# Performance work log

Measured on AMD Instinct MI355X. Metric: run time of the kernel, lower is better.

## Reference

```python
import jax, jax.numpy as jnp
import numpy as np

B, N, E, F, H, OUT = 128, 2048, 16384, 32, 64, 16


def setup_inputs() -> dict:
    key = jax.random.key(0)
    ks = jax.random.split(key, 8)
    node_features = jax.random.normal(ks[0], (B, N, F), jnp.float32)
    edge_index = jax.random.randint(ks[1], (B, 2, E), 0, N)
    n_nodes = jax.random.randint(ks[2], (B,), N // 2, N + 1)
    # prefix node mask (required for the original's index-consistency)
    node_mask = jnp.arange(N)[None, :] < n_nodes[:, None]
    glorot = lambda k, sh, fan: jax.random.normal(k, sh, jnp.float32) / np.sqrt(fan)
    return dict(
        node_features=node_features, edge_index=edge_index, node_mask=node_mask,
        W1=glorot(ks[3], (F, H), F), b1=jnp.zeros((H,), jnp.float32),
        W2=glorot(ks[4], (H, H), H), b2=jnp.zeros((H,), jnp.float32),
        aW1=glorot(ks[5], (H, H), H), ab1=jnp.zeros((H,), jnp.float32),
        aW2=glorot(ks[6], (H, OUT), H), ab2=jnp.zeros((OUT,), jnp.float32),
    )


def reference(node_features, edge_index, node_mask, W1, b1, W2, b2, aW1, ab1, aW2, ab2):
    x = node_features
    src, dst = edge_index[:, 0], edge_index[:, 1]          # [B,E] source->target
    n = node_mask.sum(-1)                                   # [B] valid nodes per graph
    max_idx = n - 1
    emask = (src <= max_idx[:, None]) & (dst <= max_idx[:, None])
    w = emask.astype(x.dtype)                               # [B,E] edge weights

    # flatten batch into one big segment space [B*N]
    offs = (jnp.arange(B, dtype=src.dtype) * N)[:, None]
    src_f = (src + offs).reshape(-1)
    dst_f = (dst + offs).reshape(-1)
    w_f = w.reshape(-1)

    # GCN normalization with self-loops (PyG GCNConv default)
    deg = jax.ops.segment_sum(w_f, dst_f, num_segments=B * N).reshape(B, N)
    deg = deg + node_mask.astype(x.dtype)                   # self-loop weight 1 on valid nodes
    dis = jnp.where(deg > 0, jax.lax.rsqrt(deg), 0.0)       # deg^{-1/2}, [B,N]
    dis_f = dis.reshape(-1)
    norm = dis_f[src_f] * dis_f[dst_f] * w_f                # [B*E]
    nmask_f = node_mask.reshape(-1).astype(x.dtype)[:, None]
    nmask = node_mask.astype(x.dtype)[..., None]

    def gcn_relu(h, W, bias):
        hW = (h @ W).reshape(B * N, -1)                     # transform first (PyG order)
        msgs = hW[src_f] * norm[:, None]                    # [B*E, H]
        agg = jax.ops.segment_sum(msgs, dst_f, num_segments=B * N)
        agg = agg + hW * ((dis * dis).reshape(-1)[:, None] * nmask_f)  # self-loop term
        out = (agg.reshape(B, N, -1) + bias) * nmask
        return jax.nn.relu(out)

    h1 = gcn_relu(x * nmask, W1, b1)
    h2 = gcn_relu(h1, W2, b2)

    # mean pool over valid nodes (zeros if empty graph)
    pooled = h2.sum(1) / jnp.maximum(n, 1)[:, None].astype(x.dtype)
    hidden = jax.nn.relu(pooled @ aW1 + ab1)
    logits = hidden @ aW2 + ab2                             # [B, OUT]
    return logits
```

## Files before the change

### kernel.cpp

```cpp
#include <hip/hip_runtime.h>
#include <hip/hip_bf16.h>

#define B 128
#define N 2048
#define E 16384
#define F 32
#define H 64
#define OUTD 16
#define CAP 16
#define NP1 (N + 1)

typedef __attribute__((ext_vector_type(8))) short bf16x8;
typedef __attribute__((ext_vector_type(4))) float f32x4;

__device__ __forceinline__ float b2f(unsigned short u) {
    return __uint_as_float(((unsigned int)u) << 16);
}
__device__ __forceinline__ unsigned short f2b(float f) {
    unsigned int x = __float_as_uint(f);
    unsigned int r = (x + 0x7FFFu + ((x >> 16) & 1u)) >> 16;
    return (unsigned short)r;
}
__device__ __forceinline__ unsigned int pack2(float a, float b) {
    return (unsigned int)f2b(a) | ((unsigned int)f2b(b) << 16);
}

__device__ __forceinline__ void unpack8(float (&a)[8], uint4 u) {
    a[0] += __uint_as_float(u.x << 16);
    a[1] += __uint_as_float(u.x & 0xffff0000u);
    a[2] += __uint_as_float(u.y << 16);
    a[3] += __uint_as_float(u.y & 0xffff0000u);
    a[4] += __uint_as_float(u.z << 16);
    a[5] += __uint_as_float(u.z & 0xffff0000u);
    a[6] += __uint_as_float(u.w << 16);
    a[7] += __uint_as_float(u.w & 0xffff0000u);
}

struct PrepArgs {
    const void* src[9];
    void* dst[9];
};

__global__ __launch_bounds__(1024) void k_build(
    const void* __restrict__ x, const int* __restrict__ eidx,
    const void* __restrict__ mask, PrepArgs pa, int* __restrict__ flags,
    int* __restrict__ n_arr, float* __restrict__ dis,
    unsigned char* __restrict__ degc, unsigned short* __restrict__ ssrc,
    int2* __restrict__ ovf, int* __restrict__ ovf_cnt,
    float* __restrict__ pooled, unsigned int* __restrict__ y_u,
    unsigned int* __restrict__ z_u) {
    __shared__ int s_cnt[N];
    __shared__ float s_fred[16];
    __shared__ int s_w[16];
    __shared__ int s_n, s_ovf, s_xbf, s_pf;
    const int b = blockIdx.x;
    const int t = threadIdx.x;
    const int bN = b * N;
    {
        const unsigned short* p = (const unsigned short*)x;
        float s = fminf(fabsf(b2f(p[t])), 1e6f);
        for (int o = 32; o > 0; o >>= 1) s += __shfl_down(s, o);
        if ((t & 63) == 0) s_fred[t >> 6] = s;
        __syncthreads();
        if (t == 0) {
            float a = 0.f;
            for (int i = 0; i < 16; i++) a += s_fred[i];
            int f = (a < 100.0f * 1024.0f) ? 1 : 0;
            s_xbf = f;
            if (b == 0) flags[0] = f;
        }
    }
    const unsigned char* mb = (const unsigned char*)mask;
    int mode;
    if (mb[0] == 0x80 && mb[1] == 0x3F) mode = 2;
    else if (mb[0] != 0 && mb[1] != 0) mode = 0;
    else if (mb[0] != 0) mode = (mb[4] != 0) ? 1 : 4;
    else mode = 3;
    int cnt = 0;
    if (mode == 0) {
        const unsigned char* r = mb + (size_t)b * N;
        for (int i = t; i < N; i += 1024) cnt += (r[i] != 0);
    } else if (mode == 1 || mode == 3) {
        const unsigned int* r = (const unsigned int*)mask + (size_t)b * N;
        for (int i = t; i < N; i += 1024) cnt += (r[i] != 0);
    } else if (mode == 2) {
        const unsigned short* r = (const unsigned short*)mask + (size_t)b * N;
        for (int i = t; i < N; i += 1024) cnt += (r[i] != 0);
    } else {
        const unsigned long long* r = (const unsigned long long*)mask + (size_t)b * N;
        for (int i = t; i < N; i += 1024) cnt += (r[i] != 0ULL);
    }
    for (int o = 32; o > 0; o >>= 1) cnt += __shfl_down(cnt, o);
    if ((t & 63) == 0) s_w[t >> 6] = cnt;
    for (int i = t; i < N; i += 1024) s_cnt[i] = 0;
    {
        const int4 iv = make_int4(0x08000800, 0x08000800, 0x08000800, 0x08000800);
        int4* sp4 = (int4*)(ssrc + (size_t)bN * CAP);
        for (int i = t; i < N * CAP / 8; i += 1024) sp4[i] = iv;
    }
    if (t < 16) y_u[((size_t)b * NP1 + N) * (F / 2) + t] = 0u;
    if (t >= 32 && t < 64) z_u[((size_t)b * NP1 + N) * (H / 2) + (t - 32)] = 0u;
    if (t == 0) s_ovf = 0;
    __syncthreads();
    if (t == 0) {
        int a = 0;
        for (int i = 0; i < 16; i++) a += s_w[i];
        s_n = a > N ? N : a;
    }
    __syncthreads();
    const int n = s_n;
    const int4* es4 = (const int4*)(eidx + (size_t)b * 2 * E);
    const int4* ed4 = es4 + E / 4;
    for (int i = t; i < E / 4; i += 1024) {
        int4 s4 = es4[i], d4 = ed4[i];
#define FILL1(SS, DD)                                                          \
        if ((unsigned)(SS) < (unsigned)n && (unsigned)(DD) < (unsigned)n) {    \
            int pos = atomicAdd(&s_cnt[DD], 1);                                \
            if (pos < CAP)                                                     \
                ssrc[((size_t)(bN + (DD))) * CAP + pos] = (unsigned short)(SS);\
            else {                                                             \
                int oi = atomicAdd(&s_ovf, 1);                                 \
                if (oi < E) ovf[(size_t)b * E + oi] = make_int2((DD), (SS));   \
            }                                                                  \
        }
        FILL1(s4.x, d4.x) FILL1(s4.y, d4.y) FILL1(s4.z, d4.z) FILL1(s4.w, d4.w)
#undef FILL1
    }
    __syncthreads();
    for (int v = t; v < N; v += 1024) {
        int c = s_cnt[v];
        dis[bN + v] = (v < n) ? rsqrtf((float)(c + 1)) : 0.0f;
        degc[bN + v] = (unsigned char)(c < CAP ? c : CAP);
    }
    if (t < H) pooled[b * H + t] = 0.0f;
    if (t == 0) { n_arr[b] = n; ovf_cnt[b] = s_ovf; }
    if (s_xbf) {
        const uint4* xp = (const uint4*)((const unsigned short*)x + (size_t)bN * F);
        for (int i = t; i < N * 4; i += 1024) {
            const int v = i >> 2;
            const int c = s_cnt[v];
            const float dv = (v < n) ? rsqrtf((float)(c + 1)) : 0.0f;
            uint4 u = xp[i];
            uint4 o;
            o.x = pack2(b2f((unsigned short)u.x) * dv, b2f((unsigned short)(u.x >> 16)) * dv);
            o.y = pack2(b2f((unsigned short)u.y) * dv, b2f((unsigned short)(u.y >> 16)) * dv);
            o.z = pack2(b2f((unsigned short)u.z) * dv, b2f((unsigned short)(u.z >> 16)) * dv);
            o.w = pack2(b2f((unsigned short)u.w) * dv, b2f((unsigned short)(u.w >> 16)) * dv);
            *(uint4*)(y_u + ((size_t)b * NP1 + v) * (F / 2) + (i & 3) * 4) = o;
        }
    } else {
        const float4* xp = (const float4*)((const float*)x + (size_t)bN * F);
        for (int i = t; i < N * 4; i += 1024) {
            const int v = i >> 2;
            const int c = s_cnt[v];
            const float dv = (v < n) ? rsqrtf((float)(c + 1)) : 0.0f;
            float4 v1 = xp[i * 2], v2 = xp[i * 2 + 1];
            uint4 o;
            o.x = pack2(v1.x * dv, v1.y * dv);
            o.y = pack2(v1.z * dv, v1.w * dv);
            o.z = pack2(v2.x * dv, v2.y * dv);
            o.w = pack2(v2.z * dv, v2.w * dv);
            *(uint4*)(y_u + ((size_t)b * NP1 + v) * (F / 2) + (i & 3) * 4) = o;
        }
    }
    if (b >= 1 && b <= 8) {
        int sz;
        switch (b) {
            case 1: sz = F * H; break;
            case 2: sz = H; break;
            case 3: sz = H * H; break;
            case 4: sz = H; break;
            case 5: sz = H * H; break;
            case 6: sz = H; break;
            case 7: sz = H * OUTD; break;
            default: sz = OUTD; break;
        }
        const int K = sz < 1024 ? sz : 1024;
        const unsigned short* p = (const unsigned short*)pa.src[b];
        float s = (t < K) ? fminf(fabsf(b2f(p[t])), 1e6f) : 0.f;
        for (int o = 32; o > 0; o >>= 1) s += __shfl_down(s, o);
        __syncthreads();
        if ((t & 63) == 0) s_fred[t >> 6] = s;
        __syncthreads();
        if (t == 0) {
            float a = 0.f;
            for (int i = 0; i < 16; i++) a += s_fred[i];
            s_pf = (a < 100.0f * (float)K) ? 1 : 0;
        }
        __syncthreads();
        const int fl = s_pf;
        auto rd = [&](int i) -> float {
            return fl ? b2f(((const unsigned short*)pa.src[b])[i])
                      : ((const float*)pa.src[b])[i];
        };
        if (b == 1) {
            unsigned short* dst = (unsigned short*)pa.dst[b];
            for (int i = t; i < F * H; i += 1024) {
                int k = i >> 6, n2 = i & 63;
                dst[n2 * 40 + k] = f2b(rd(i));
            }
        } else if (b == 3) {
            unsigned short* dst = (unsigned short*)pa.dst[b];
            for (int i = t; i < H * H; i += 1024) {
                int k = i >> 6, n2 = i & 63;
                dst[n2 * 72 + k] = f2b(rd(i));
            }
        } else {
            float* dst = (float*)pa.dst[b];
            for (int i = t; i < sz; i += 1024) dst[i] = rd(i);
        }
    }
}

__global__ __launch_bounds__(256) void k_agg_gemm1(
    const unsigned int* __restrict__ y_u, const float* __restrict__ dis,
    const unsigned char* __restrict__ degc, const unsigned short* __restrict__ ssrc,
    const int2* __restrict__ ovf, const int* __restrict__ ovf_cnt,
    const unsigned short* __restrict__ w1t, const float* __restrict__ b1f,
    unsigned short* __restrict__ zs) {
    __shared__ unsigned short s_e[64 * CAP];
    __shared__ unsigned char s_dg[64];
    __shared__ float s_dv[64];
    __shared__ float s_b1[64];
    __shared__ __align__(16) unsigned short s_w1t[64 * 40];
    __shared__ __align__(16) unsigned short s_a1[64 * 40];
    const int bid = blockIdx.x;
    const int b = (bid & 7) + ((bid >> 8) << 3);
    const int v0 = ((bid >> 3) & 31) * 64;
    const int t = threadIdx.x;
    const int bN = b * N;
    if (t < 128) ((int4*)s_e)[t] = ((const int4*)(ssrc + (size_t)(bN + v0) * CAP))[t];
    if (t >= 128 && t < 144)
        ((unsigned int*)s_dg)[t - 128] = ((const unsigned int*)(degc + bN + v0))[t - 128];
    if (t >= 192) s_dv[t - 192] = dis[bN + v0 + (t - 192)];
    if (t >= 144 && t < 208) s_b1[t - 144] = b1f[t - 144];
    for (int i = t; i < 320; i += 256) ((int4*)s_w1t)[i] = ((const int4*)w1t)[i];
    __syncthreads();
    const int lane = t & 63;
    const int w = t >> 6;
    const int oc = ovf_cnt[b];
    const unsigned int* yb = y_u + (size_t)b * NP1 * (F / 2);
    {
        const int nn = w * 16 + (lane >> 2);
        const int v = v0 + nn;
        const int cu = (lane & 3) * 4;
        int md = s_dg[w * 16 + (lane & 15)];
        int m2;
        m2 = __shfl_xor(md, 1); md = md > m2 ? md : m2;
        m2 = __shfl_xor(md, 2); md = md > m2 ? md : m2;
        m2 = __shfl_xor(md, 4); md = md > m2 ? md : m2;
        m2 = __shfl_xor(md, 8); md = md > m2 ? md : m2;
        const unsigned short* ep = &s_e[nn * CAP];
        float a[8] = {0.f, 0.f, 0.f, 0.f, 0.f, 0.f, 0.f, 0.f};
        uint4 cur = *(const uint4*)(yb + (size_t)v * (F / 2) + cu);
        uint4 nxt = *(const uint4*)(yb + (size_t)ep[0] * (F / 2) + cu);
        for (int s = 0; s < md; s++) {
            int sn = s + 1; sn = sn > CAP - 1 ? CAP - 1 : sn;
            uint4 n2 = *(const uint4*)(yb + (size_t)ep[sn] * (F / 2) + cu);
            unpack8(a, cur);
            cur = nxt; nxt = n2;
        }
        unpack8(a, cur);
        if (oc > 0) {
            const int2* ob = ovf + (size_t)b * E;
            for (int j = 0; j < oc; j++) {
                int2 o = ob[j];
                if (o.x == v) {
                    uint4 u4 = *(const uint4*)(yb + (size_t)o.y * (F / 2) + cu);
                    unpack8(a, u4);
                }
            }
        }
        const float dv = s_dv[nn];
        uint4 ov;
        ov.x = pack2(a[0] * dv, a[1] * dv);
        ov.y = pack2(a[2] * dv, a[3] * dv);
        ov.z = pack2(a[4] * dv, a[5] * dv);
        ov.w = pack2(a[6] * dv, a[7] * dv);
        *(uint4*)((unsigned int*)s_a1 + nn * 20 + cu) = ov;
    }
    __syncthreads();
    const int quad = lane >> 4;
    const int f2 = lane & 15;
    const int m0 = w * 16;
    bf16x8 af = *(const bf16x8*)&s_a1[(m0 + f2) * 40 + quad * 8];
    float dvr[4];
#pragma unroll
    for (int r = 0; r < 4; r++) dvr[r] = s_dv[m0 + quad * 4 + r];
#pragma unroll
    for (int nt = 0; nt < 4; nt++) {
        bf16x8 bf = *(const bf16x8*)&s_w1t[(nt * 16 + f2) * 40 + quad * 8];
        f32x4 acc = {0.f, 0.f, 0.f, 0.f};
        acc = __builtin_amdgcn_mfma_f32_16x16x32_bf16(af, bf, acc, 0, 0, 0);
        float bb = s_b1[nt * 16 + f2];
#pragma unroll
        for (int r = 0; r < 4; r++) {
            int row = m0 + quad * 4 + r;
            float val = dvr[r] * fmaxf(acc[r] + bb, 0.0f);
            zs[((size_t)b * NP1 + v0 + row) * H + nt * 16 + f2] = f2b(val);
        }
    }
}

__global__ __launch_bounds__(256) void k_agg_gemm2_pool(
    const unsigned int* __restrict__ z_u, const float* __restrict__ dis,
    const unsigned char* __restrict__ degc, const unsigned short* __restrict__ ssrc,
    const int2* __restrict__ ovf, const int* __restrict__ ovf_cnt,
    const unsigned short* __restrict__ w2t, const float* __restrict__ b2f_,
    float* __restrict__ pooled) {
    __shared__ unsigned short s_e[64 * CAP];
    __shared__ unsigned char s_dg[64];
    __shared__ float s_dv[64];
    __shared__ float s_b2[64];
    __shared__ __align__(16) unsigned short s_w2t[64 * 72];
    __shared__ __align__(16) unsigned short s_a2[64 * 72];
    __shared__ float s_pool[4][64];
    const int bid = blockIdx.x;
    const int b = (bid & 7) + ((bid >> 8) << 3);
    const int v0 = ((bid >> 3) & 31) * 64;
    const int t = threadIdx.x;
    const int bN = b * N;
    if (t < 128) ((int4*)s_e)[t] = ((const int4*)(ssrc + (size_t)(bN + v0) * CAP))[t];
    if (t >= 128 && t < 144)
        ((unsigned int*)s_dg)[t - 128] = ((const unsigned int*)(degc + bN + v0))[t - 128];
    if (t >= 192) s_dv[t - 192] = dis[bN + v0 + (t - 192)];
    if (t >= 144 && t < 208) s_b2[t - 144] = b2f_[t - 144];
    for (int i = t; i < 576; i += 256) ((int4*)s_w2t)[i] = ((const int4*)w2t)[i];
    __syncthreads();
    const int lane = t & 63;
    const int w = t >> 6;
    const int oc = ovf_cnt[b];
    const unsigned int* zb = z_u + (size_t)b * NP1 * (H / 2);
#pragma unroll
    for (int g = 0; g < 2; g++) {
        const int nn = w * 16 + g * 8 + (lane >> 3);
        const int v = v0 + nn;
        const int cu = (lane & 7) * 4;
        int md = s_dg[w * 16 + g * 8 + (lane & 7)];
        int m2;
        m2 = __shfl_xor(md, 1); md = md > m2 ? md : m2;
        m2 = __shfl_xor(md, 2); md = md > m2 ? md : m2;
        m2 = __shfl_xor(md, 4); md = md > m2 ? md : m2;
        const unsigned short* ep = &s_e[nn * CAP];
        float a[8] = {0.f, 0.f, 0.f, 0.f, 0.f, 0.f, 0.f, 0.f};
        uint4 cur = *(const uint4*)(zb + (size_t)v * (H / 2) + cu);
        uint4 nxt = *(const uint4*)(zb + (size_t)ep[0] * (H / 2) + cu);
        for (int s = 0; s < md; s++) {
            int sn = s + 1; sn = sn > CAP - 1 ? CAP - 1 : sn;
            uint4 n2 = *(const uint4*)(zb + (size_t)ep[sn] * (H / 2) + cu);
            unpack8(a, cur);
            cur = nxt; nxt = n2;
        }
        unpack8(a, cur);
        if (oc > 0) {
            const int2* ob = ovf + (size_t)b * E;
            for (int j = 0; j < oc; j++) {
                int2 o = ob[j];
                if (o.x == v) {
                    uint4 u4 = *(const uint4*)(zb + (size_t)o.y * (H / 2) + cu);
                    unpack8(a, u4);
                }
            }
        }
        const float dv = s_dv[nn];
        uint4 ov;
        ov.x = pack2(a[0] * dv, a[1] * dv);
        ov.y = pack2(a[2] * dv, a[3] * dv);
        ov.z = pack2(a[4] * dv, a[5] * dv);
        ov.w = pack2(a[6] * dv, a[7] * dv);
        *(uint4*)((unsigned int*)s_a2 + nn * 36 + cu) = ov;
    }
    __syncthreads();
    const int quad = lane >> 4;
    const int f2 = lane & 15;
    const int m0 = w * 16;
    bf16x8 af0 = *(const bf16x8*)&s_a2[(m0 + f2) * 72 + quad * 8];
    bf16x8 af1 = *(const bf16x8*)&s_a2[(m0 + f2) * 72 + 32 + quad * 8];
    float dvr[4];
#pragma unroll
    for (int r = 0; r < 4; r++) dvr[r] = s_dv[m0 + quad * 4 + r];
#pragma unroll
    for (int nt = 0; nt < 4; nt++) {
        bf16x8 bf0 = *(const bf16x8*)&s_w2t[(nt * 16 + f2) * 72 + quad * 8];
        bf16x8 bf1 = *(const bf16x8*)&s_w2t[(nt * 16 + f2) * 72 + 32 + quad * 8];
        f32x4 acc = {0.f, 0.f, 0.f, 0.f};
        acc = __builtin_amdgcn_mfma_f32_16x16x32_bf16(af0, bf0, acc, 0, 0, 0);
        acc = __builtin_amdgcn_mfma_f32_16x16x32_bf16(af1, bf1, acc, 0, 0, 0);
        float bb = s_b2[nt * 16 + f2];
        float ps = 0.f;
#pragma unroll
        for (int r = 0; r < 4; r++)
            ps += (dvr[r] > 0.0f) ? fmaxf(acc[r] + bb, 0.0f) : 0.0f;
        ps += __shfl_xor(ps, 16);
        ps += __shfl_xor(ps, 32);
        if (quad == 0) s_pool[w][nt * 16 + f2] = ps;
    }
    __syncthreads();
    if (t < H)
        atomicAdd(&pooled[b * H + t],
                  s_pool[0][t] + s_pool[1][t] + s_pool[2][t] + s_pool[3][t]);
}

__global__ __launch_bounds__(64) void k_mlp(
    const float* __restrict__ pooled, const int* __restrict__ n_arr,
    const float* __restrict__ aW1, const float* __restrict__ ab1,
    const float* __restrict__ aW2, const float* __restrict__ ab2,
    const int* __restrict__ flags, void* __restrict__ out) {
    const int b = blockIdx.x;
    const int t = threadIdx.x;
    __shared__ float p[64];
    __shared__ float hid[64];
    int n = n_arr[b];
    if (n < 1) n = 1;
    p[t] = pooled[b * H + t] / (float)n;
    __syncthreads();
    float acc = ab1[t];
    for (int j = 0; j < 64; j++) acc += p[j] * aW1[j * 64 + t];
    hid[t] = fmaxf(acc, 0.0f);
    __syncthreads();
    if (t < 16) {
        float a2 = ab2[t];
        for (int j = 0; j < 64; j++) a2 += hid[j] * aW2[j * 16 + t];
        if (flags[0]) ((unsigned short*)out)[b * OUTD + t] = f2b(a2);
        else          ((float*)out)[b * OUTD + t] = a2;
    }
}

extern "C" void kernel_launch(void* const* d_in, const int* in_sizes, int n_in,
                              void* d_out, int out_size, void* d_ws, size_t ws_size,
                              hipStream_t stream) {
    const void* x    = d_in[0];
    const int*  eidx = (const int*)d_in[1];
    const void* mask = d_in[2];

    char* ws = (char*)d_ws;
    size_t off = 0;
    auto alloc = [&](size_t bytes) -> void* {
        void* p = ws + off;
        off += (bytes + 255) & ~(size_t)255;
        return p;
    };
    int*   flags   = (int*)alloc(16 * sizeof(int));
    unsigned short* w1t = (unsigned short*)alloc(64 * 40 * 2);
    unsigned short* w2t = (unsigned short*)alloc(64 * 72 * 2);
    float* b1f     = (float*)alloc(H * sizeof(float));
    float* b2f_    = (float*)alloc(H * sizeof(float));
    float* aW1f    = (float*)alloc(H * H * sizeof(float));
    float* ab1f    = (float*)alloc(H * sizeof(float));
    float* aW2f    = (float*)alloc(H * OUTD * sizeof(float));
    float* ab2f    = (float*)alloc(OUTD * sizeof(float));
    int*   n_arr   = (int*)alloc(B * sizeof(int));
    float* dis     = (float*)alloc((size_t)B * N * sizeof(float));
    unsigned char*  degc = (unsigned char*)alloc((size_t)B * N);
    unsigned short* ssrc = (unsigned short*)alloc((size_t)B * N * CAP * 2);
    int2*  ovf     = (int2*)alloc((size_t)B * E * sizeof(int2));
    int*   ovf_cnt = (int*)alloc(B * sizeof(int));
    float* pooled  = (float*)alloc((size_t)B * H * sizeof(float));
    unsigned int* y_u = (unsigned int*)alloc((size_t)B * NP1 * (F / 2) * 4);
    unsigned int* z_u = (unsigned int*)alloc((size_t)B * NP1 * (H / 2) * 4);

    PrepArgs pa;
    pa.src[0] = x;        pa.dst[0] = pooled;
    pa.src[1] = d_in[3];  pa.dst[1] = w1t;
    pa.src[2] = d_in[4];  pa.dst[2] = b1f;
    pa.src[3] = d_in[5];  pa.dst[3] = w2t;
    pa.src[4] = d_in[6];  pa.dst[4] = b2f_;
    pa.src[5] = d_in[7];  pa.dst[5] = aW1f;
    pa.src[6] = d_in[8];  pa.dst[6] = ab1f;
    pa.src[7] = d_in[9];  pa.dst[7] = aW2f;
    pa.src[8] = d_in[10]; pa.dst[8] = ab2f;

    k_build<<<B, 1024, 0, stream>>>(x, eidx, mask, pa, flags, n_arr, dis, degc,
                                    ssrc, ovf, ovf_cnt, pooled, y_u, z_u);
    k_agg_gemm1<<<B * 32, 256, 0, stream>>>(y_u, dis, degc, ssrc, ovf, ovf_cnt,
                                            w1t, b1f, (unsigned short*)z_u);
    k_agg_gemm2_pool<<<B * 32, 256, 0, stream>>>(z_u, dis, degc, ssrc, ovf,
                                                 ovf_cnt, w2t, b2f_, pooled);
    k_mlp<<<B, 64, 0, stream>>>(pooled, n_arr, aW1f, ab1f, aW2f, ab2f, flags, d_out);
}
```

Measured before the change: 165.0 us.

## Drop prescaled feature buffer and sentinel fill; apply source norm during layer-1 gather

The build kernel no longer writes a dis-prescaled bf16 copy of the node features or fills the neighbor-list buffer with sentinel indices. Layer 1 now reads bf16 input directly, or a plain converted copy when the input is fp32, and multiplies each gathered neighbor by its dis value with FMA, masking padding slots by degree. Layer 2 masks unused slots to the zero row explicitly, and the edge loads are unrolled and issued up front. This removes a large write pass in the build kernel at the cost of an extra scalar dis load per neighbor in the layer-1 gather.

```diff
diff --git a/kernel.cpp b/kernel.cpp
--- a/kernel.cpp
+++ b/kernel.cpp
@@ -25,7 +25,7 @@
     return (unsigned int)f2b(a) | ((unsigned int)f2b(b) << 16);
 }
 
-__device__ __forceinline__ void unpack8(float (&a)[8], uint4 u) {
+__device__ __forceinline__ void add8(float (&a)[8], uint4 u) {
     a[0] += __uint_as_float(u.x << 16);
     a[1] += __uint_as_float(u.x & 0xffff0000u);
     a[2] += __uint_as_float(u.y << 16);
@@ -35,6 +35,16 @@
     a[6] += __uint_as_float(u.w << 16);
     a[7] += __uint_as_float(u.w & 0xffff0000u);
 }
+__device__ __forceinline__ void fma8(float (&a)[8], uint4 u, float w) {
+    a[0] = fmaf(__uint_as_float(u.x << 16), w, a[0]);
+    a[1] = fmaf(__uint_as_float(u.x & 0xffff0000u), w, a[1]);
+    a[2] = fmaf(__uint_as_float(u.y << 16), w, a[2]);
+    a[3] = fmaf(__uint_as_float(u.y & 0xffff0000u), w, a[3]);
+    a[4] = fmaf(__uint_as_float(u.z << 16), w, a[4]);
+    a[5] = fmaf(__uint_as_float(u.z & 0xffff0000u), w, a[5]);
+    a[6] = fmaf(__uint_as_float(u.w << 16), w, a[6]);
+    a[7] = fmaf(__uint_as_float(u.w & 0xffff0000u), w, a[7]);
+}
 
 struct PrepArgs {
     const void* src[9];
@@ -47,7 +57,7 @@
     int* __restrict__ n_arr, float* __restrict__ dis,
     unsigned char* __restrict__ degc, unsigned short* __restrict__ ssrc,
     int2* __restrict__ ovf, int* __restrict__ ovf_cnt,
-    float* __restrict__ pooled, unsigned int* __restrict__ y_u,
+    float* __restrict__ pooled, unsigned int* __restrict__ xconv,
     unsigned int* __restrict__ z_u) {
     __shared__ int s_cnt[N];
     __shared__ float s_fred[16];
@@ -93,12 +103,6 @@
     for (int o = 32; o > 0; o >>= 1) cnt += __shfl_down(cnt, o);
     if ((t & 63) == 0) s_w[t >> 6] = cnt;
     for (int i = t; i < N; i += 1024) s_cnt[i] = 0;
-    {
-        const int4 iv = make_int4(0x08000800, 0x08000800, 0x08000800, 0x08000800);
-        int4* sp4 = (int4*)(ssrc + (size_t)bN * CAP);
-        for (int i = t; i < N * CAP / 8; i += 1024) sp4[i] = iv;
-    }
-    if (t < 16) y_u[((size_t)b * NP1 + N) * (F / 2) + t] = 0u;
     if (t >= 32 && t < 64) z_u[((size_t)b * NP1 + N) * (H / 2) + (t - 32)] = 0u;
     if (t == 0) s_ovf = 0;
     __syncthreads();
@@ -111,8 +115,15 @@
     const int n = s_n;
     const int4* es4 = (const int4*)(eidx + (size_t)b * 2 * E);
     const int4* ed4 = es4 + E / 4;
-    for (int i = t; i < E / 4; i += 1024) {
-        int4 s4 = es4[i], d4 = ed4[i];
+    int4 sv[4], dv4[4];
+#pragma unroll
+    for (int k = 0; k < 4; k++) {
+        sv[k] = es4[t + k * 1024];
+        dv4[k] = ed4[t + k * 1024];
+    }
+#pragma unroll
+    for (int k = 0; k < 4; k++) {
+        int4 s4 = sv[k], d4 = dv4[k];
 #define FILL1(SS, DD)                                                          \
         if ((unsigned)(SS) < (unsigned)n && (unsigned)(DD) < (unsigned)n) {    \
             int pos = atomicAdd(&s_cnt[DD], 1);                                \
@@ -134,33 +145,12 @@
     }
     if (t < H) pooled[b * H + t] = 0.0f;
     if (t == 0) { n_arr[b] = n; ovf_cnt[b] = s_ovf; }
-    if (s_xbf) {
-        const uint4* xp = (const uint4*)((const unsigned short*)x + (size_t)bN * F);
-        for (int i = t; i < N * 4; i += 1024) {
-            const int v = i >> 2;
-            const int c = s_cnt[v];
-            const float dv = (v < n) ? rsqrtf((float)(c + 1)) : 0.0f;
-            uint4 u = xp[i];
-            uint4 o;
-            o.x = pack2(b2f((unsigned short)u.x) * dv, b2f((unsigned short)(u.x >> 16)) * dv);
-            o.y = pack2(b2f((unsigned short)u.y) * dv, b2f((unsigned short)(u.y >> 16)) * dv);
-            o.z = pack2(b2f((unsigned short)u.z) * dv, b2f((unsigned short)(u.z >> 16)) * dv);
-            o.w = pack2(b2f((unsigned short)u.w) * dv, b2f((unsigned short)(u.w >> 16)) * dv);
-            *(uint4*)(y_u + ((size_t)b * NP1 + v) * (F / 2) + (i & 3) * 4) = o;
-        }
-    } else {
+    if (!s_xbf) {
         const float4* xp = (const float4*)((const float*)x + (size_t)bN * F);
-        for (int i = t; i < N * 4; i += 1024) {
-            const int v = i >> 2;
-            const int c = s_cnt[v];
-            const float dv = (v < n) ? rsqrtf((float)(c + 1)) : 0.0f;
-            float4 v1 = xp[i * 2], v2 = xp[i * 2 + 1];
-            uint4 o;
-            o.x = pack2(v1.x * dv, v1.y * dv);
-            o.y = pack2(v1.z * dv, v1.w * dv);
-            o.z = pack2(v2.x * dv, v2.y * dv);
-            o.w = pack2(v2.z * dv, v2.w * dv);
-            *(uint4*)(y_u + ((size_t)b * NP1 + v) * (F / 2) + (i & 3) * 4) = o;
+        uint2* yp = (uint2*)(xconv + (size_t)bN * (F / 2));
+        for (int i = t; i < N * F / 4; i += 1024) {
+            float4 v4 = xp[i];
+            yp[i] = make_uint2(pack2(v4.x, v4.y), pack2(v4.z, v4.w));
         }
     }
     if (b >= 1 && b <= 8) {
@@ -213,7 +203,8 @@
 }
 
 __global__ __launch_bounds__(256) void k_agg_gemm1(
-    const unsigned int* __restrict__ y_u, const float* __restrict__ dis,
+    const void* __restrict__ x, const unsigned int* __restrict__ xconv,
+    const int* __restrict__ flags, const float* __restrict__ dis,
     const unsigned char* __restrict__ degc, const unsigned short* __restrict__ ssrc,
     const int2* __restrict__ ovf, const int* __restrict__ ovf_cnt,
     const unsigned short* __restrict__ w1t, const float* __restrict__ b1f,
@@ -239,11 +230,15 @@
     const int lane = t & 63;
     const int w = t >> 6;
     const int oc = ovf_cnt[b];
-    const unsigned int* yb = y_u + (size_t)b * NP1 * (F / 2);
+    const unsigned int* yb =
+        (flags[0] ? (const unsigned int*)x : xconv) + (size_t)bN * (F / 2);
+    const float* disb = dis + bN;
     {
         const int nn = w * 16 + (lane >> 2);
         const int v = v0 + nn;
         const int cu = (lane & 3) * 4;
+        const int dg = s_dg[nn];
+        const float dv = s_dv[nn];
         int md = s_dg[w * 16 + (lane & 15)];
         int m2;
         m2 = __shfl_xor(md, 1); md = md > m2 ? md : m2;
@@ -252,32 +247,38 @@
         m2 = __shfl_xor(md, 8); md = md > m2 ? md : m2;
         const unsigned short* ep = &s_e[nn * CAP];
         float a[8] = {0.f, 0.f, 0.f, 0.f, 0.f, 0.f, 0.f, 0.f};
-        uint4 cur = *(const uint4*)(yb + (size_t)v * (F / 2) + cu);
-        uint4 nxt = *(const uint4*)(yb + (size_t)ep[0] * (F / 2) + cu);
+        uint4 rs = *(const uint4*)(yb + (size_t)v * (F / 2) + cu);
+        int i0 = ep[0] & (N - 1);
+        int i1 = ep[1] & (N - 1);
+        uint4 r0 = *(const uint4*)(yb + (size_t)i0 * (F / 2) + cu);
+        float w0p = disb[i0];
+        uint4 r1 = *(const uint4*)(yb + (size_t)i1 * (F / 2) + cu);
+        float w1p = disb[i1];
+        fma8(a, rs, dv);
         for (int s = 0; s < md; s++) {
-            int sn = s + 1; sn = sn > CAP - 1 ? CAP - 1 : sn;
-            uint4 n2 = *(const uint4*)(yb + (size_t)ep[sn] * (F / 2) + cu);
-            unpack8(a, cur);
-            cur = nxt; nxt = n2;
-        }
-        unpack8(a, cur);
+            int sn = s + 2; sn = sn > CAP - 1 ? CAP - 1 : sn;
+            int i2 = ep[sn] & (N - 1);
+            uint4 r2 = *(const uint4*)(yb + (size_t)i2 * (F / 2) + cu);
+            float w2p = disb[i2];
+            fma8(a, r0, s < dg ? w0p : 0.0f);
+            r0 = r1; w0p = w1p; r1 = r2; w1p = w2p;
+        }
         if (oc > 0) {
             const int2* ob = ovf + (size_t)b * E;
             for (int j = 0; j < oc; j++) {
                 int2 o = ob[j];
                 if (o.x == v) {
                     uint4 u4 = *(const uint4*)(yb + (size_t)o.y * (F / 2) + cu);
-                    unpack8(a, u4);
+                    fma8(a, u4, disb[o.y]);
                 }
             }
         }
-        const float dv = s_dv[nn];
-        uint4 ov;
-        ov.x = pack2(a[0] * dv, a[1] * dv);
-        ov.y = pack2(a[2] * dv, a[3] * dv);
-        ov.z = pack2(a[4] * dv, a[5] * dv);
-        ov.w = pack2(a[6] * dv, a[7] * dv);
-        *(uint4*)((unsigned int*)s_a1 + nn * 20 + cu) = ov;
+        uint4 ovv;
+        ovv.x = pack2(a[0] * dv, a[1] * dv);
+        ovv.y = pack2(a[2] * dv, a[3] * dv);
+        ovv.z = pack2(a[4] * dv, a[5] * dv);
+        ovv.w = pack2(a[6] * dv, a[7] * dv);
+        *(uint4*)((unsigned int*)s_a1 + nn * 20 + cu) = ovv;
     }
     __syncthreads();
     const int quad = lane >> 4;
@@ -336,6 +337,7 @@
         const int nn = w * 16 + g * 8 + (lane >> 3);
         const int v = v0 + nn;
         const int cu = (lane & 7) * 4;
+        const int dg = s_dg[nn];
         int md = s_dg[w * 16 + g * 8 + (lane & 7)];
         int m2;
         m2 = __shfl_xor(md, 1); md = md > m2 ? md : m2;
@@ -344,31 +346,33 @@
         const unsigned short* ep = &s_e[nn * CAP];
         float a[8] = {0.f, 0.f, 0.f, 0.f, 0.f, 0.f, 0.f, 0.f};
         uint4 cur = *(const uint4*)(zb + (size_t)v * (H / 2) + cu);
-        uint4 nxt = *(const uint4*)(zb + (size_t)ep[0] * (H / 2) + cu);
+        int i0 = (0 < dg) ? (ep[0] & (N - 1)) : N;
+        uint4 nxt = *(const uint4*)(zb + (size_t)i0 * (H / 2) + cu);
         for (int s = 0; s < md; s++) {
             int sn = s + 1; sn = sn > CAP - 1 ? CAP - 1 : sn;
-            uint4 n2 = *(const uint4*)(zb + (size_t)ep[sn] * (H / 2) + cu);
-            unpack8(a, cur);
+            int i2 = (s + 1 < dg) ? (ep[sn] & (N - 1)) : N;
+            uint4 n2 = *(const uint4*)(zb + (size_t)i2 * (H / 2) + cu);
+            add8(a, cur);
             cur = nxt; nxt = n2;
         }
-        unpack8(a, cur);
+        add8(a, cur);
         if (oc > 0) {
             const int2* ob = ovf + (size_t)b * E;
             for (int j = 0; j < oc; j++) {
                 int2 o = ob[j];
                 if (o.x == v) {
                     uint4 u4 = *(const uint4*)(zb + (size_t)o.y * (H / 2) + cu);
-                    unpack8(a, u4);
+                    add8(a, u4);
                 }
             }
         }
         const float dv = s_dv[nn];
-        uint4 ov;
-        ov.x = pack2(a[0] * dv, a[1] * dv);
-        ov.y = pack2(a[2] * dv, a[3] * dv);
-        ov.z = pack2(a[4] * dv, a[5] * dv);
-        ov.w = pack2(a[6] * dv, a[7] * dv);
-        *(uint4*)((unsigned int*)s_a2 + nn * 36 + cu) = ov;
+        uint4 ovv;
+        ovv.x = pack2(a[0] * dv, a[1] * dv);
+        ovv.y = pack2(a[2] * dv, a[3] * dv);
+        ovv.z = pack2(a[4] * dv, a[5] * dv);
+        ovv.w = pack2(a[6] * dv, a[7] * dv);
+        *(uint4*)((unsigned int*)s_a2 + nn * 36 + cu) = ovv;
     }
     __syncthreads();
     const int quad = lane >> 4;
@@ -456,7 +460,7 @@
     int2*  ovf     = (int2*)alloc((size_t)B * E * sizeof(int2));
     int*   ovf_cnt = (int*)alloc(B * sizeof(int));
     float* pooled  = (float*)alloc((size_t)B * H * sizeof(float));
-    unsigned int* y_u = (unsigned int*)alloc((size_t)B * NP1 * (F / 2) * 4);
+    unsigned int* xconv = (unsigned int*)alloc((size_t)B * N * (F / 2) * 4);
     unsigned int* z_u = (unsigned int*)alloc((size_t)B * NP1 * (H / 2) * 4);
 
     PrepArgs pa;
@@ -471,9 +475,10 @@
     pa.src[8] = d_in[10]; pa.dst[8] = ab2f;
 
     k_build<<<B, 1024, 0, stream>>>(x, eidx, mask, pa, flags, n_arr, dis, degc,
-                                    ssrc, ovf, ovf_cnt, pooled, y_u, z_u);
-    k_agg_gemm1<<<B * 32, 256, 0, stream>>>(y_u, dis, degc, ssrc, ovf, ovf_cnt,
-                                            w1t, b1f, (unsigned short*)z_u);
+                                    ssrc, ovf, ovf_cnt, pooled, xconv, z_u);
+    k_agg_gemm1<<<B * 32, 256, 0, stream>>>(x, xconv, flags, dis, degc, ssrc,
+                                            ovf, ovf_cnt, w1t, b1f,
+                                            (unsigned short*)z_u);
     k_agg_gemm2_pool<<<B * 32, 256, 0, stream>>>(z_u, dis, degc, ssrc, ovf,
                                                  ovf_cnt, w2t, b2f_, pooled);
     k_mlp<<<B, 64, 0, stream>>>(pooled, n_arr, aW1f, ab1f, aW2f, ab2f, flags, d_out);
```

Result: no change. 165.6 us (+0.4%).
